# Optimization experiments

Measured on AMD Instinct MI355X. Metric: run time of the kernel, lower is better.

The kernel has to match this reference:

```python
import jax, jax.numpy as jnp
import numpy as np

B = 64            # graphs per batch
NODES_PER_GRAPH = 1008  # 12 snapshots * 84 nodes
N = B * NODES_PER_GRAPH # 64512 total nodes
E = N * 16              # ~1M edges
SNAP = 12
SEG = 84
D_IN = 84
D_H = 128
EPS_BN = 1e-5


def setup_inputs() -> dict:
    key = jax.random.key(0)
    ks = jax.random.split(key, 20)
    s = 0.05  # small init scale for numerical sanity
    return {
        "x": jax.random.normal(ks[0], (N, D_IN), jnp.float32),
        "edge_index": jax.random.randint(ks[1], (2, E), 0, N, jnp.int64),
        "w1": jax.random.normal(ks[2], (D_IN, D_H), jnp.float32) * s,
        "b1": jax.random.normal(ks[3], (D_H,), jnp.float32) * s,
        "w2": jax.random.normal(ks[4], (D_H, D_H), jnp.float32) * s,
        "b2": jax.random.normal(ks[5], (D_H,), jnp.float32) * s,
        "pe": jax.random.normal(ks[6], (NODES_PER_GRAPH, D_H), jnp.float32) * s,
        "wf1": jax.random.normal(ks[7], (SNAP * 4 * D_H, 512), jnp.float32) * s,
        "bf1": jax.random.normal(ks[8], (512,), jnp.float32) * s,
        "g1": jnp.ones((512,), jnp.float32),
        "be1": jnp.zeros((512,), jnp.float32),
        "wf2": jax.random.normal(ks[9], (512, 32), jnp.float32) * s,
        "bf2": jax.random.normal(ks[10], (32,), jnp.float32) * s,
        "g2": jnp.ones((32,), jnp.float32),
        "be2": jnp.zeros((32,), jnp.float32),
        "wf3": jax.random.normal(ks[11], (32, 2), jnp.float32) * s,
        "bf3": jax.random.normal(ks[12], (2,), jnp.float32) * s,
    }


def _batch_norm(h, g, b):
    # training-mode BN: biased batch statistics, eps=1e-5 (torch default)
    mu = jnp.mean(h, axis=0)
    var = jnp.var(h, axis=0)
    return (h - mu) * jax.lax.rsqrt(var + EPS_BN) * g + b


def reference(x, edge_index, w1, b1, w2, b2, pe, wf1, bf1, g1, be1,
              wf2, bf2, g2, be2, wf3, bf3):
    src, dst = edge_index[0], edge_index[1]
    n = x.shape[0]
    b = n // NODES_PER_GRAPH

    # GINConv (eps=0, sum aggregation): h = Linear(x + sum_{j->i} x_j)
    agg1 = jax.ops.segment_sum(x[src], dst, num_segments=n)
    h1 = (x + agg1) @ w1 + b1                      # [N,128]
    agg2 = jax.ops.segment_sum(h1[src], dst, num_segments=n)
    h2 = (h1 + agg2) @ w2 + b2                     # [N,128]

    # positional encoding + full self-attention per graph (1008 tokens)
    h2 = h2.reshape(b, NODES_PER_GRAPH, D_H) + pe  # [B,1008,128]
    score = jnp.einsum('bqd,bkd->bqk', h2, h2) / np.sqrt(float(D_H))
    attn = jax.nn.softmax(score, axis=-1)
    ctx = jnp.einsum('bqk,bkd->bqd', attn, h2)     # [B,1008,128]

    # segmented max/mean pooling: blocks of 84 nodes, 12 snapshots per graph
    h1s = h1.reshape(b, SNAP, SEG, D_H)
    h2s = ctx.reshape(b, SNAP, SEG, D_H)
    feat = jnp.concatenate([
        jnp.max(h1s, axis=2), jnp.mean(h1s, axis=2),
        jnp.max(h2s, axis=2), jnp.mean(h2s, axis=2),
    ], axis=-1)                                    # [B,12,512]
    feat = feat.reshape(b, SNAP * 4 * D_H)         # [B,6144]

    # MLP head (dropout = identity at eval; BN in training-stat mode)
    out = _batch_norm(jax.nn.silu(feat @ wf1 + bf1), g1, be1)
    out = _batch_norm(jax.nn.silu(out @ wf2 + bf2), g2, be2)
    out = jax.nn.softmax(out @ wf3 + bf3, axis=1)  # [B,2]
    return out
```

## Files before the change

### kernel.cpp

```cpp
#include <hip/hip_runtime.h>
#include <math.h>

#define N_NODES 64512
#define DIN 84
#define XHP 96
#define KP 96
#define USP 104
#define DH 128
#define NPG 1008
#define BG 64
#define NSNAP 12
#define NSEG 84
#define NEDGE (N_NODES * 16)
#define DEGCAP 64
#define NBUCK 252
#define EPB 4096
#define BCAP 4608
#define ATT_SCALE 0.08838834764831845f

typedef __bf16 bf16_t;
typedef __bf16 bf16x8 __attribute__((ext_vector_type(8)));
typedef __bf16 bf16x4 __attribute__((ext_vector_type(4)));
typedef float f32x4 __attribute__((ext_vector_type(4)));
typedef _Float16 f16_t;
typedef _Float16 f16x4 __attribute__((ext_vector_type(4)));
typedef _Float16 f16x8 __attribute__((ext_vector_type(8)));

__device__ __forceinline__ f32x4 up4(f16x4 v) {
    return (f32x4){(float)v[0], (float)v[1], (float)v[2], (float)v[3]};
}

__global__ __launch_bounds__(256) void cvt_xh(const float* __restrict__ x,
                                              f16_t* __restrict__ xh,
                                              int* __restrict__ bucketTail) {
    int t = blockIdx.x * 256 + threadIdx.x;
    if (t < N_NODES * 21) {
        int node = t / 21;
        int c = t - node * 21;
        f32x4 v = *(const f32x4*)(x + (size_t)node * DIN + c * 4);
        f16x4 o;
        o[0] = (f16_t)v[0]; o[1] = (f16_t)v[1];
        o[2] = (f16_t)v[2]; o[3] = (f16_t)v[3];
        *(f16x4*)(xh + (size_t)node * XHP + c * 4) = o;
    }
    if (t * 4 < NBUCK) {
        int4 z = {0, 0, 0, 0};
        *(int4*)(bucketTail + t * 4) = z;
    }
}

__global__ __launch_bounds__(256) void epart(const int* __restrict__ src,
                                             const int* __restrict__ dst,
                                             int* __restrict__ bucketTail,
                                             unsigned int* __restrict__ rec) {
    __shared__ int lcnt[NBUCK];
    __shared__ int gbase[NBUCK];
    int tid = threadIdx.x;
    int e0 = blockIdx.x * EPB;
    for (int i = tid; i < NBUCK; i += 256) lcnt[i] = 0;
    __syncthreads();

    unsigned int r[16];
    unsigned short lp[16];
    unsigned short bk[16];
#pragma unroll
    for (int i = 0; i < 16; i++) {
        int e = e0 + tid + i * 256;
        int s = src[e], d = dst[e];
        r[i] = ((unsigned int)d << 16) | (unsigned int)s;
        int b = d >> 8;
        bk[i] = (unsigned short)b;
        lp[i] = (unsigned short)atomicAdd(&lcnt[b], 1);
    }
    __syncthreads();
    for (int i = tid; i < NBUCK; i += 256)
        gbase[i] = atomicAdd(&bucketTail[i], lcnt[i]);
    __syncthreads();
#pragma unroll
    for (int i = 0; i < 16; i++) {
        int b = bk[i];
        int g = gbase[b] + lp[i];
        if (g < BCAP) rec[(size_t)b * BCAP + g] = r[i];
    }
}

__global__ __launch_bounds__(256) void ebuild(const unsigned int* __restrict__ rec,
                                              const int* __restrict__ bucketTail,
                                              int* __restrict__ cnt,
                                              unsigned short* __restrict__ eidx) {
    __shared__ unsigned short stage[256 * 72];
    __shared__ int rb8[256 * 8];
    int tid = threadIdx.x;
    int b = blockIdx.x;
#pragma unroll
    for (int i = 0; i < 8; i++) rb8[tid + i * 256] = 0;
    __syncthreads();

    int n = min(bucketTail[b], BCAP);
    const unsigned int* rbp = rec + (size_t)b * BCAP;
    for (int i = tid; i < n; i += 256) {
        unsigned int rv = rbp[i];
        int ld = (rv >> 16) & 255;
        int rng = (rv & 0xffffu) >> 13;
        atomicAdd(&rb8[ld * 8 + rng], 1);
    }
    __syncthreads();
    {
        int s = 0;
#pragma unroll
        for (int r = 0; r < 8; r++) {
            int c = rb8[tid * 8 + r];
            rb8[tid * 8 + r] = s;
            s += c;
        }
        cnt[b * 256 + tid] = s;
    }
    __syncthreads();
    for (int i = tid; i < n; i += 256) {
        unsigned int rv = rbp[i];
        int ld = (rv >> 16) & 255;
        int rng = (rv & 0xffffu) >> 13;
        int p = atomicAdd(&rb8[ld * 8 + rng], 1);
        if (p < DEGCAP) stage[ld * 72 + p] = (unsigned short)(rv & 0xffffu);
    }
    __syncthreads();

    uint4* op = (uint4*)(eidx + (size_t)b * 256 * DEGCAP);
#pragma unroll
    for (int i = 0; i < 8; i++) {
        int ch = tid + i * 256;
        int node = ch >> 3, e0 = (ch & 7) << 3;
        op[ch] = *(const uint4*)&stage[node * 72 + e0];
    }
}

__global__ __launch_bounds__(128) void prep_w12(const float* __restrict__ w1,
                                                const float* __restrict__ w2,
                                                const float* __restrict__ b1,
                                                f16_t* __restrict__ w1hT,
                                                f16_t* __restrict__ w12hT,
                                                float* __restrict__ bvec) {
    __shared__ float rowv[DH];
    int r = blockIdx.x;
    int j = threadIdx.x;
    const float* srcv = (r < DIN) ? (w1 + (size_t)r * DH) : b1;
    rowv[j] = srcv[j];
    __syncthreads();
    float acc = 0.f;
#pragma unroll 4
    for (int k = 0; k < DH; k++) acc += rowv[k] * w2[k * DH + j];
    if (r < DIN) {
        w12hT[j * KP + r] = (f16_t)acc;
        w1hT[j * KP + r] = (f16_t)w1[(size_t)r * DH + j];
    } else {
        bvec[j] = acc;
        for (int k = DIN; k < KP; k++) {
            w1hT[j * KP + k] = (f16_t)0.f;
            w12hT[j * KP + k] = (f16_t)0.f;
        }
    }
}

__global__ __launch_bounds__(512) void gin1(const float* __restrict__ x,
                                            const f16_t* __restrict__ xh,
                                            const int* __restrict__ cnt,
                                            const unsigned short* __restrict__ eidx,
                                            const f16_t* __restrict__ w1hT,
                                            const float* __restrict__ b1,
                                            float* __restrict__ h1,
                                            f16_t* __restrict__ zh) {
    __shared__ f16_t us[32][USP];
    int n0 = blockIdx.x * 32;
    int tid = threadIdx.x;
    int grp = tid >> 4;
    int gl = tid & 15;
    int node = n0 + grp;
    int s = node * DEGCAP;
    int e = s + min(cnt[node], DEGCAP);
    bool has2 = gl < 5;

    const float* xn = x + (size_t)node * DIN;
    f32x4 a0 = *(const f32x4*)(xn + gl * 4);
    f32x4 a1 = has2 ? *(const f32x4*)(xn + 64 + gl * 4) : (f32x4){0.f, 0.f, 0.f, 0.f};

    int i = s;
    for (; i + 4 <= e; i += 4) {
        const f16_t* p0 = xh + (size_t)eidx[i] * XHP + gl * 4;
        const f16_t* p1 = xh + (size_t)eidx[i + 1] * XHP + gl * 4;
        const f16_t* p2 = xh + (size_t)eidx[i + 2] * XHP + gl * 4;
        const f16_t* p3 = xh + (size_t)eidx[i + 3] * XHP + gl * 4;
        a0 += up4(*(const f16x4*)p0) + up4(*(const f16x4*)p1) +
              up4(*(const f16x4*)p2) + up4(*(const f16x4*)p3);
        if (has2) {
            a1 += up4(*(const f16x4*)(p0 + 64)) + up4(*(const f16x4*)(p1 + 64)) +
                  up4(*(const f16x4*)(p2 + 64)) + up4(*(const f16x4*)(p3 + 64));
        }
    }
    for (; i < e; i++) {
        const f16_t* p0 = xh + (size_t)eidx[i] * XHP + gl * 4;
        a0 += up4(*(const f16x4*)p0);
        if (has2) a1 += up4(*(const f16x4*)(p0 + 64));
    }

    f16x4 z0;
    z0[0] = (f16_t)a0[0]; z0[1] = (f16_t)a0[1];
    z0[2] = (f16_t)a0[2]; z0[3] = (f16_t)a0[3];
    *(f16x4*)(zh + (size_t)node * XHP + gl * 4) = z0;
    *(f16x4*)&us[grp][gl * 4] = z0;
    if (has2) {
        f16x4 z1;
        z1[0] = (f16_t)a1[0]; z1[1] = (f16_t)a1[1];
        z1[2] = (f16_t)a1[2]; z1[3] = (f16_t)a1[3];
        *(f16x4*)(zh + (size_t)node * XHP + 64 + gl * 4) = z1;
        *(f16x4*)&us[grp][64 + gl * 4] = z1;
    }
    if (gl >= 5 && gl < 8) {
        f16x4 zz = {(f16_t)0.f, (f16_t)0.f, (f16_t)0.f, (f16_t)0.f};
        *(f16x4*)&us[grp][64 + gl * 4] = zz;
    }
    __syncthreads();

    int wv = tid >> 6, lane = tid & 63;
    int l15 = lane & 15, quad = lane >> 4;
    int dim = wv * 16 + l15;
    f32x4 acc[2];
    acc[0] = (f32x4){0.f, 0.f, 0.f, 0.f};
    acc[1] = (f32x4){0.f, 0.f, 0.f, 0.f};
#pragma unroll
    for (int ks = 0; ks < 3; ks++) {
        f16x8 bW = *(const f16x8*)(w1hT + (size_t)dim * KP + ks * 32 + quad * 8);
        f16x8 aU0 = *(const f16x8*)&us[l15][ks * 32 + quad * 8];
        f16x8 aU1 = *(const f16x8*)&us[16 + l15][ks * 32 + quad * 8];
        acc[0] = __builtin_amdgcn_mfma_f32_16x16x32_f16(aU0, bW, acc[0], 0, 0, 0);
        acc[1] = __builtin_amdgcn_mfma_f32_16x16x32_f16(aU1, bW, acc[1], 0, 0, 0);
    }
    float bias = b1[dim];
#pragma unroll
    for (int tm = 0; tm < 2; tm++) {
        int nb = n0 + tm * 16 + quad * 4;
#pragma unroll
        for (int r = 0; r < 4; r++)
            h1[(size_t)(nb + r) * DH + dim] = acc[tm][r] + bias;
    }
}

__global__ __launch_bounds__(512) void gin2(const f16_t* __restrict__ zh,
                                            const int* __restrict__ cnt,
                                            const unsigned short* __restrict__ eidx,
                                            const f16_t* __restrict__ w12hT,
                                            const float* __restrict__ bvec,
                                            const float* __restrict__ b2,
                                            const float* __restrict__ pe,
                                            bf16_t* __restrict__ h2bf,
                                            bf16_t* __restrict__ h2T) {
    __shared__ f16_t us[32][USP];
    __shared__ float sdeg[32];
    int n0 = blockIdx.x * 32;
    int tid = threadIdx.x;
    int grp = tid >> 4;
    int gl = tid & 15;
    int node = n0 + grp;
    int dg = min(cnt[node], DEGCAP);
    int s = node * DEGCAP;
    int e = s + dg;
    bool has2 = gl < 5;
    if (gl == 0) sdeg[grp] = (float)(1 + dg);

    const f16_t* zn = zh + (size_t)node * XHP;
    f32x4 a0 = up4(*(const f16x4*)(zn + gl * 4));
    f32x4 a1 = has2 ? up4(*(const f16x4*)(zn + 64 + gl * 4)) : (f32x4){0.f, 0.f, 0.f, 0.f};

    int i = s;
    for (; i + 4 <= e; i += 4) {
        const f16_t* p0 = zh + (size_t)eidx[i] * XHP + gl * 4;
        const f16_t* p1 = zh + (size_t)eidx[i + 1] * XHP + gl * 4;
        const f16_t* p2 = zh + (size_t)eidx[i + 2] * XHP + gl * 4;
        const f16_t* p3 = zh + (size_t)eidx[i + 3] * XHP + gl * 4;
        a0 += up4(*(const f16x4*)p0) + up4(*(const f16x4*)p1) +
              up4(*(const f16x4*)p2) + up4(*(const f16x4*)p3);
        if (has2) {
            a1 += up4(*(const f16x4*)(p0 + 64)) + up4(*(const f16x4*)(p1 + 64)) +
                  up4(*(const f16x4*)(p2 + 64)) + up4(*(const f16x4*)(p3 + 64));
        }
    }
    for (; i < e; i++) {
        const f16_t* p0 = zh + (size_t)eidx[i] * XHP + gl * 4;
        a0 += up4(*(const f16x4*)p0);
        if (has2) a1 += up4(*(const f16x4*)(p0 + 64));
    }
    f16x4 u0;
    u0[0] = (f16_t)a0[0]; u0[1] = (f16_t)a0[1];
    u0[2] = (f16_t)a0[2]; u0[3] = (f16_t)a0[3];
    *(f16x4*)&us[grp][gl * 4] = u0;
    if (has2) {
        f16x4 u1;
        u1[0] = (f16_t)a1[0]; u1[1] = (f16_t)a1[1];
        u1[2] = (f16_t)a1[2]; u1[3] = (f16_t)a1[3];
        *(f16x4*)&us[grp][64 + gl * 4] = u1;
    }
    if (gl >= 5 && gl < 8) {
        f16x4 zz = {(f16_t)0.f, (f16_t)0.f, (f16_t)0.f, (f16_t)0.f};
        *(f16x4*)&us[grp][64 + gl * 4] = zz;
    }
    __syncthreads();

    int wv = tid >> 6, lane = tid & 63;
    int l15 = lane & 15, quad = lane >> 4;
    int dim = wv * 16 + l15;
    f32x4 acc[2];
    acc[0] = (f32x4){0.f, 0.f, 0.f, 0.f};
    acc[1] = (f32x4){0.f, 0.f, 0.f, 0.f};
#pragma unroll
    for (int ks = 0; ks < 3; ks++) {
        f16x8 bW = *(const f16x8*)(w12hT + (size_t)dim * KP + ks * 32 + quad * 8);
        f16x8 aU0 = *(const f16x8*)&us[l15][ks * 32 + quad * 8];
        f16x8 aU1 = *(const f16x8*)&us[16 + l15][ks * 32 + quad * 8];
        acc[0] = __builtin_amdgcn_mfma_f32_16x16x32_f16(aU0, bW, acc[0], 0, 0, 0);
        acc[1] = __builtin_amdgcn_mfma_f32_16x16x32_f16(aU1, bW, acc[1], 0, 0, 0);
    }

    float bb = b2[dim];
    float bv = bvec[dim];
#pragma unroll
    for (int tm = 0; tm < 2; tm++) {
        int nb = n0 + tm * 16 + quad * 4;
        int bg = nb / NPG;
        int pos = nb - bg * NPG;
        bf16x4 tv;
#pragma unroll
        for (int r = 0; r < 4; r++) {
            float v = acc[tm][r] + bb + sdeg[tm * 16 + quad * 4 + r] * bv +
                      pe[(size_t)(pos + r) * DH + dim];
            bf16_t vb = (bf16_t)v;
            h2bf[(size_t)(nb + r) * DH + dim] = vb;
            tv[r] = vb;
        }
        *(bf16x4*)(h2T + ((size_t)bg * DH + dim) * NPG + pos) = tv;
    }
}

#define QTILE 256
#define KTILE 64
#define KS_PITCH 152
#define KT_PITCH 88
#define PS_PITCH 88
#define KSSZ 9728
#define KTSZ 11264
#define BUFSZ (KSSZ + KTSZ)
#define PS2_OFF (2 * BUFSZ)

__global__ __launch_bounds__(512, 1) void attn_mfma(const bf16_t* __restrict__ h2bf,
                                                    const bf16_t* __restrict__ h2T,
                                                    float* __restrict__ ctx) {
    __shared__ __align__(16) bf16_t smem[PS2_OFF + QTILE * PS_PITCH];

    int tid = threadIdx.x;
    int wv = tid >> 6, lane = tid & 63;
    int l15 = lane & 15, quad = lane >> 4;
    int idx = blockIdx.x;
    int xcd = idx & 7;
    int qt = (idx >> 3) & 3;
    int b = (idx >> 5) * 8 + xcd;
    const bf16_t* hb = h2bf + (size_t)b * NPG * DH;
    const bf16_t* hbT = h2T + (size_t)b * DH * NPG;

    bf16x8 bQ[2][4];
#pragma unroll
    for (int set = 0; set < 2; set++) {
        int qrow_frag = qt * QTILE + wv * 32 + set * 16 + l15;
        int qsrc = (qrow_frag < NPG) ? qrow_frag : 0;
#pragma unroll
        for (int kb = 0; kb < 4; kb++)
            bQ[set][kb] = *(const bf16x8*)(hb + (size_t)qsrc * DH + kb * 32 + quad * 8);
    }

    float m0 = -1e30f, li0 = 0.0f;
    float m1 = -1e30f, li1 = 0.0f;
    f32x4 O[2][8];
#pragma unroll
    for (int t = 0; t < 8; t++) {
        O[0][t] = (f32x4){0.f, 0.f, 0.f, 0.f};
        O[1][t] = (f32x4){0.f, 0.f, 0.f, 0.f};
    }

    uint4 rK[2], rT[2];
#define LOADR(KT_)                                                              \
    {                                                                           \
        int kt_ = (KT_);                                                        \
        _Pragma("unroll")                                                       \
        for (int i = 0; i < 2; i++) {                                           \
            int c = tid + i * 512;                                              \
            int row = c >> 4, seg = c & 15;                                     \
            int key = kt_ * KTILE + row;                                        \
            uint4 v = {0u, 0u, 0u, 0u};                                         \
            if (key < NPG) v = *(const uint4*)(hb + (size_t)key * DH + seg * 8);\
            rK[i] = v;                                                          \
        }                                                                       \
        _Pragma("unroll")                                                       \
        for (int i = 0; i < 2; i++) {                                           \
            int c = tid + i * 512;                                              \
            int dim = c >> 3, kc = c & 7;                                       \
            int key0 = kt_ * KTILE + kc * 8;                                    \
            uint4 v = {0u, 0u, 0u, 0u};                                         \
            if (key0 < NPG) v = *(const uint4*)(hbT + (size_t)dim * NPG + key0);\
            rT[i] = v;                                                          \
        }                                                                       \
    }
#define DRAIN(BUFOFF_)                                                          \
    {                                                                           \
        int bo_ = (BUFOFF_);                                                    \
        _Pragma("unroll")                                                       \
        for (int i = 0; i < 2; i++) {                                           \
            int c = tid + i * 512;                                              \
            int row = c >> 4, seg = c & 15;                                     \
            *(uint4*)&smem[bo_ + row * KS_PITCH + seg * 8] = rK[i];             \
        }                                                                       \
        _Pragma("unroll")                                                       \
        for (int i = 0; i < 2; i++) {                                           \
            int c = tid + i * 512;                                              \
            int dim = c >> 3, kc = c & 7;                                       \
            *(uint4*)&smem[bo_ + KSSZ + dim * KT_PITCH + kc * 8] = rT[i];       \
        }                                                                       \
    }

    LOADR(0);
    DRAIN(0);
    LOADR(1);
    __syncthreads();

    for (int kt = 0; kt < 16; kt++) {
        int bo = (kt & 1) * BUFSZ;
        if (kt < 15) DRAIN(((kt + 1) & 1) * BUFSZ);
        if (kt < 14) LOADR(kt + 2);

        f32x4 S[2][4];
#pragma unroll
        for (int nt = 0; nt < 4; nt++) {
            S[0][nt] = (f32x4){0.f, 0.f, 0.f, 0.f};
            S[1][nt] = (f32x4){0.f, 0.f, 0.f, 0.f};
#pragma unroll
            for (int kb = 0; kb < 4; kb++) {
                bf16x8 aK = *(const bf16x8*)&smem[bo + (nt * 16 + l15) * KS_PITCH + kb * 32 + quad * 8];
                S[0][nt] = __builtin_amdgcn_mfma_f32_16x16x32_bf16(aK, bQ[0][kb], S[0][nt], 0, 0, 0);
                S[1][nt] = __builtin_amdgcn_mfma_f32_16x16x32_bf16(aK, bQ[1][kb], S[1][nt], 0, 0, 0);
            }
        }

        float pmax0 = -1e30f, pmax1 = -1e30f;
#pragma unroll
        for (int nt = 0; nt < 4; nt++) {
            bool valid = (kt * KTILE + nt * 16) < NPG;
#pragma unroll
            for (int r = 0; r < 4; r++) {
                float v0 = valid ? S[0][nt][r] * ATT_SCALE : -1e30f;
                float v1 = valid ? S[1][nt][r] * ATT_SCALE : -1e30f;
                S[0][nt][r] = v0;
                S[1][nt][r] = v1;
                pmax0 = fmaxf(pmax0, v0);
                pmax1 = fmaxf(pmax1, v1);
            }
        }
        pmax0 = fmaxf(pmax0, __shfl_xor(pmax0, 16));
        pmax0 = fmaxf(pmax0, __shfl_xor(pmax0, 32));
        pmax1 = fmaxf(pmax1, __shfl_xor(pmax1, 16));
        pmax1 = fmaxf(pmax1, __shfl_xor(pmax1, 32));
        float newm0 = fmaxf(m0, pmax0);
        float newm1 = fmaxf(m1, pmax1);

        float alpha0 = 1.0f, alpha1 = 1.0f;
        if (!__all((newm0 == m0) && (newm1 == m1))) {
            alpha0 = __expf(m0 - newm0);
            alpha1 = __expf(m1 - newm1);
            float a00 = __shfl(alpha0, quad * 4 + 0);
            float a01 = __shfl(alpha0, quad * 4 + 1);
            float a02 = __shfl(alpha0, quad * 4 + 2);
            float a03 = __shfl(alpha0, quad * 4 + 3);
            float a10 = __shfl(alpha1, quad * 4 + 0);
            float a11 = __shfl(alpha1, quad * 4 + 1);
            float a12 = __shfl(alpha1, quad * 4 + 2);
            float a13 = __shfl(alpha1, quad * 4 + 3);
#pragma unroll
            for (int t = 0; t < 8; t++) {
                O[0][t][0] *= a00; O[0][t][1] *= a01; O[0][t][2] *= a02; O[0][t][3] *= a03;
                O[1][t][0] *= a10; O[1][t][1] *= a11; O[1][t][2] *= a12; O[1][t][3] *= a13;
            }
        }
        m0 = newm0;
        m1 = newm1;

        float psum0 = 0.f, psum1 = 0.f;
#pragma unroll
        for (int nt = 0; nt < 4; nt++) {
            bf16x4 pk0, pk1;
#pragma unroll
            for (int r = 0; r < 4; r++) {
                float p0 = __expf(S[0][nt][r] - newm0);
                float p1 = __expf(S[1][nt][r] - newm1);
                psum0 += p0;
                psum1 += p1;
                pk0[r] = (bf16_t)p0;
                pk1[r] = (bf16_t)p1;
            }
            *(bf16x4*)&smem[PS2_OFF + (wv * 32 + l15) * PS_PITCH + nt * 16 + quad * 4] = pk0;
            *(bf16x4*)&smem[PS2_OFF + (wv * 32 + 16 + l15) * PS_PITCH + nt * 16 + quad * 4] = pk1;
        }
        psum0 += __shfl_xor(psum0, 16);
        psum0 += __shfl_xor(psum0, 32);
        psum1 += __shfl_xor(psum1, 16);
        psum1 += __shfl_xor(psum1, 32);
        li0 = li0 * alpha0 + psum0;
        li1 = li1 * alpha1 + psum1;

#pragma unroll
        for (int kb2 = 0; kb2 < 2; kb2++) {
            bf16x8 aP0 = *(const bf16x8*)&smem[PS2_OFF + (wv * 32 + l15) * PS_PITCH + kb2 * 32 + quad * 8];
            bf16x8 aP1 = *(const bf16x8*)&smem[PS2_OFF + (wv * 32 + 16 + l15) * PS_PITCH + kb2 * 32 + quad * 8];
#pragma unroll
            for (int t = 0; t < 8; t++) {
                bf16x8 bV = *(const bf16x8*)&smem[bo + KSSZ + (t * 16 + l15) * KT_PITCH + kb2 * 32 + quad * 8];
                O[0][t] = __builtin_amdgcn_mfma_f32_16x16x32_bf16(aP0, bV, O[0][t], 0, 0, 0);
                O[1][t] = __builtin_amdgcn_mfma_f32_16x16x32_bf16(aP1, bV, O[1][t], 0, 0, 0);
            }
        }

        __syncthreads();
    }
#undef LOADR
#undef DRAIN

    float invl0[4], invl1[4];
#pragma unroll
    for (int r = 0; r < 4; r++) {
        invl0[r] = 1.0f / __shfl(li0, quad * 4 + r);
        invl1[r] = 1.0f / __shfl(li1, quad * 4 + r);
    }
    float* cb = ctx + (size_t)b * NPG * DH;
#pragma unroll
    for (int t = 0; t < 8; t++)
#pragma unroll
        for (int r = 0; r < 4; r++) {
            int qrow0 = qt * QTILE + wv * 32 + quad * 4 + r;
            int qrow1 = qrow0 + 16;
            if (qrow0 < NPG) cb[(size_t)qrow0 * DH + t * 16 + l15] = O[0][t][r] * invl0[r];
            if (qrow1 < NPG) cb[(size_t)qrow1 * DH + t * 16 + l15] = O[1][t][r] * invl1[r];
        }
}

__global__ __launch_bounds__(128) void pooling(const float* __restrict__ h1,
                                               const float* __restrict__ ctx,
                                               const float* __restrict__ bf1,
                                               float* __restrict__ feat,
                                               float* __restrict__ y1raw) {
    int bs = blockIdx.x;
    int d = threadIdx.x;
    if (bs < 256) {
        int i = bs * 128 + d;
        y1raw[i] = bf1[i & 511];
    }
    int base = bs * NSEG;
    float mx1 = -1e30f, sm1 = 0.f, mx2 = -1e30f, sm2 = 0.f;
    for (int n = 0; n < NSEG; n++) {
        float v1 = h1[(size_t)(base + n) * DH + d];
        mx1 = fmaxf(mx1, v1);
        sm1 += v1;
        float v2 = ctx[(size_t)(base + n) * DH + d];
        mx2 = fmaxf(mx2, v2);
        sm2 += v2;
    }
    const float invs = 1.0f / NSEG;
    feat[bs * 512 + d] = mx1;
    feat[bs * 512 + 128 + d] = sm1 * invs;
    feat[bs * 512 + 256 + d] = mx2;
    feat[bs * 512 + 384 + d] = sm2 * invs;
}

#define MLP1_KCH 96
__global__ __launch_bounds__(256) void mlp1_splitk(const float* __restrict__ feat,
                                                   const float* __restrict__ wf1,
                                                   float* __restrict__ y1raw) {
    __shared__ float fl[64][MLP1_KCH];
    int k0 = blockIdx.y * MLP1_KCH;
    int tid = threadIdx.x;
    for (int c = tid; c < 64 * MLP1_KCH; c += 256) {
        int row = c / MLP1_KCH;
        int kk = c - row * MLP1_KCH;
        fl[row][kk] = feat[(size_t)row * 6144 + k0 + kk];
    }
    __syncthreads();
    int col = blockIdx.x * 128 + (tid & 127);
    int rbase = (tid >> 7) * 32;
    float acc[32];
#pragma unroll
    for (int r = 0; r < 32; r++) acc[r] = 0.f;
    for (int kg = 0; kg < MLP1_KCH; kg += 4) {
        float w0 = wf1[(size_t)(k0 + kg + 0) * 512 + col];
        float w1 = wf1[(size_t)(k0 + kg + 1) * 512 + col];
        float w2 = wf1[(size_t)(k0 + kg + 2) * 512 + col];
        float w3 = wf1[(size_t)(k0 + kg + 3) * 512 + col];
#pragma unroll
        for (int r = 0; r < 32; r++) {
            float4 f = *(const float4*)&fl[rbase + r][kg];
            acc[r] += f.x * w0 + f.y * w1 + f.z * w2 + f.w * w3;
        }
    }
#pragma unroll
    for (int r = 0; r < 32; r++)
        atomicAdd(&y1raw[(size_t)(rbase + r) * 512 + col], acc[r]);
}

__global__ __launch_bounds__(1024) void head_tail(const float* __restrict__ y1raw,
                                                  const float* __restrict__ g1,
                                                  const float* __restrict__ be1,
                                                  const float* __restrict__ wf2,
                                                  const float* __restrict__ bf2,
                                                  const float* __restrict__ g2,
                                                  const float* __restrict__ be2,
                                                  const float* __restrict__ wf3,
                                                  const float* __restrict__ bf3,
                                                  float* __restrict__ out) {
    __shared__ float sscale[512];
    __shared__ float sshift[512];
    __shared__ float zsm[64][68];
    __shared__ float y2sm[64][33];
    __shared__ float scale2[32], shift2[32];

    int tid = threadIdx.x;

    if (tid < 512) {
        float s = 0.f, s2 = 0.f;
        for (int b = 0; b < 64; b++) {
            float v = y1raw[b * 512 + tid];
            float h = v / (1.0f + __expf(-v));
            s += h;
            s2 += h * h;
        }
        float mu = s * (1.0f / 64.0f);
        float var = s2 * (1.0f / 64.0f) - mu * mu;
        float sc = rsqrtf(var + 1e-5f) * g1[tid];
        sscale[tid] = sc;
        sshift[tid] = be1[tid] - mu * sc;
    }
    __syncthreads();

    int b0 = tid >> 5;
    int b1 = b0 + 32;
    int j2 = tid & 31;
    float acc0 = bf2[j2], acc1 = acc0;
    for (int kc = 0; kc < 8; kc++) {
        __syncthreads();
#pragma unroll
        for (int c = 0; c < 4; c++) {
            int lin = tid + c * 1024;
            int bb = lin >> 6;
            int kk = lin & 63;
            int k = kc * 64 + kk;
            float v = y1raw[bb * 512 + k];
            float h = v / (1.0f + __expf(-v));
            zsm[bb][kk] = h * sscale[k] + sshift[k];
        }
        __syncthreads();
        for (int kk = 0; kk < 64; kk++) {
            float wv = wf2[(kc * 64 + kk) * 32 + j2];
            acc0 += zsm[b0][kk] * wv;
            acc1 += zsm[b1][kk] * wv;
        }
    }
    y2sm[b0][j2] = acc0;
    y2sm[b1][j2] = acc1;
    __syncthreads();

    if (tid < 32) {
        float s = 0.f, s2 = 0.f;
        for (int b = 0; b < 64; b++) {
            float h = y2sm[b][tid];
            float hs = h / (1.0f + __expf(-h));
            s += hs;
            s2 += hs * hs;
        }
        float mu = s * (1.0f / 64.0f);
        float var = s2 * (1.0f / 64.0f) - mu * mu;
        float sc = rsqrtf(var + 1e-5f) * g2[tid];
        scale2[tid] = sc;
        shift2[tid] = be2[tid] - mu * sc;
    }
    __syncthreads();

    if (tid < 64) {
        float l0 = bf3[0], l1 = bf3[1];
        for (int k = 0; k < 32; k++) {
            float h = y2sm[tid][k];
            float hs = h / (1.0f + __expf(-h));
            float v = hs * scale2[k] + shift2[k];
            l0 += v * wf3[k * 2 + 0];
            l1 += v * wf3[k * 2 + 1];
        }
        float m = fmaxf(l0, l1);
        float e0 = __expf(l0 - m), e1 = __expf(l1 - m);
        float inv = 1.0f / (e0 + e1);
        out[tid * 2 + 0] = e0 * inv;
        out[tid * 2 + 1] = e1 * inv;
    }
}

extern "C" void kernel_launch(void* const* d_in, const int* in_sizes, int n_in,
                              void* d_out, int out_size, void* d_ws, size_t ws_size,
                              hipStream_t stream) {
    const float* x   = (const float*)d_in[0];
    const int*   ei  = (const int*)d_in[1];
    const float* w1  = (const float*)d_in[2];
    const float* b1  = (const float*)d_in[3];
    const float* w2  = (const float*)d_in[4];
    const float* b2  = (const float*)d_in[5];
    const float* pe  = (const float*)d_in[6];
    const float* wf1 = (const float*)d_in[7];
    const float* bf1 = (const float*)d_in[8];
    const float* g1  = (const float*)d_in[9];
    const float* be1 = (const float*)d_in[10];
    const float* wf2 = (const float*)d_in[11];
    const float* bf2 = (const float*)d_in[12];
    const float* g2  = (const float*)d_in[13];
    const float* be2 = (const float*)d_in[14];
    const float* wf3 = (const float*)d_in[15];
    const float* bf3 = (const float*)d_in[16];
    float* out = (float*)d_out;

    const int* srcp = ei;
    const int* dstp = ei + NEDGE;

    float* ws = (float*)d_ws;
    size_t off = 0;
    float* h1   = ws + off; off += (size_t)N_NODES * DH;
    float* ctxb = ws + off; off += (size_t)N_NODES * DH;
    float* feat = ws + off; off += (size_t)BG * NSNAP * 512;
    bf16_t* h2bf = (bf16_t*)(ws + off); off += (size_t)N_NODES * DH / 2;
    bf16_t* h2T  = (bf16_t*)(ws + off); off += (size_t)N_NODES * DH / 2;
    f16_t* zh    = (f16_t*)(ws + off);  off += (size_t)N_NODES * XHP / 2;
    f16_t* xh    = (f16_t*)(ws + off);  off += (size_t)N_NODES * XHP / 2;
    float* y1raw = ws + off; off += 64 * 512;
    f16_t* w1hT  = (f16_t*)(ws + off);  off += (size_t)DH * KP / 2;
    f16_t* w12hT = (f16_t*)(ws + off);  off += (size_t)DH * KP / 2;
    float* bvec  = ws + off; off += DH;
    int* bucketTail = (int*)(ws + off); off += NBUCK;
    int* cnt  = (int*)(ws + off); off += N_NODES;
    unsigned int* rec = (unsigned int*)(ws + off); off += (size_t)NBUCK * BCAP;
    unsigned short* eidx = (unsigned short*)(ws + off);

    cvt_xh<<<(N_NODES * 21 + 255) / 256, 256, 0, stream>>>(x, xh, bucketTail);
    prep_w12<<<DIN + 1, 128, 0, stream>>>(w1, w2, b1, w1hT, w12hT, bvec);
    epart<<<NEDGE / EPB, 256, 0, stream>>>(srcp, dstp, bucketTail, rec);
    ebuild<<<NBUCK, 256, 0, stream>>>(rec, bucketTail, cnt, eidx);

    gin1<<<N_NODES / 32, 512, 0, stream>>>(x, xh, cnt, eidx, w1hT, b1, h1, zh);
    gin2<<<N_NODES / 32, 512, 0, stream>>>(zh, cnt, eidx, w12hT, bvec, b2, pe, h2bf, h2T);
    attn_mfma<<<BG * 4, 512, 0, stream>>>(h2bf, h2T, ctxb);
    pooling<<<BG * NSNAP, 128, 0, stream>>>(h1, ctxb, bf1, feat, y1raw);
    mlp1_splitk<<<dim3(4, 64), 256, 0, stream>>>(feat, wf1, y1raw);
    head_tail<<<1, 1024, 0, stream>>>(y1raw, g1, be1, wf2, bf2, g2, be2, wf3, bf3, out);
}
```

Measured before the change: 360.8 us.

## Split single-block MLP head into BN-stats, per-row MLP2, and tail kernels

The single 1024-thread head kernel is replaced by three kernels. One computes the first BN scale and shift over 4 blocks. One runs the 512x32 layer with one block per batch row. The last does the second BN and softmax. This spreads the serial head work across more CUs, at the cost of two extra kernel launches and global round-trips for the intermediate scale, shift and y2 buffers.

```diff
diff --git a/kernel.cpp b/kernel.cpp
--- a/kernel.cpp
+++ b/kernel.cpp
@@ -608,65 +608,70 @@
         atomicAdd(&y1raw[(size_t)(rbase + r) * 512 + col], acc[r]);
 }
 
-__global__ __launch_bounds__(1024) void head_tail(const float* __restrict__ y1raw,
-                                                  const float* __restrict__ g1,
-                                                  const float* __restrict__ be1,
-                                                  const float* __restrict__ wf2,
-                                                  const float* __restrict__ bf2,
-                                                  const float* __restrict__ g2,
-                                                  const float* __restrict__ be2,
-                                                  const float* __restrict__ wf3,
-                                                  const float* __restrict__ bf3,
-                                                  float* __restrict__ out) {
-    __shared__ float sscale[512];
-    __shared__ float sshift[512];
-    __shared__ float zsm[64][68];
+__global__ __launch_bounds__(128) void bn1s(const float* __restrict__ y1raw,
+                                            const float* __restrict__ g1,
+                                            const float* __restrict__ be1,
+                                            float* __restrict__ sscale,
+                                            float* __restrict__ sshift) {
+    int f = blockIdx.x * 128 + threadIdx.x;
+    float s = 0.f, s2 = 0.f;
+#pragma unroll 8
+    for (int b = 0; b < 64; b++) {
+        float v = y1raw[b * 512 + f];
+        float h = v / (1.0f + __expf(-v));
+        s += h;
+        s2 += h * h;
+    }
+    float mu = s * (1.0f / 64.0f);
+    float var = s2 * (1.0f / 64.0f) - mu * mu;
+    float sc = rsqrtf(var + 1e-5f) * g1[f];
+    sscale[f] = sc;
+    sshift[f] = be1[f] - mu * sc;
+}
+
+__global__ __launch_bounds__(256) void mlp2k(const float* __restrict__ y1raw,
+                                             const float* __restrict__ sscale,
+                                             const float* __restrict__ sshift,
+                                             const float* __restrict__ wf2,
+                                             const float* __restrict__ bf2,
+                                             float* __restrict__ y2raw) {
+    __shared__ float zrow[512];
+    __shared__ float part[8][33];
+    int b = blockIdx.x;
+    int tid = threadIdx.x;
+    for (int k = tid; k < 512; k += 256) {
+        float v = y1raw[b * 512 + k];
+        float h = v / (1.0f + __expf(-v));
+        zrow[k] = h * sscale[k] + sshift[k];
+    }
+    __syncthreads();
+    int j = tid & 31, s = tid >> 5;
+    float acc = 0.f;
+    int k0 = s * 64;
+#pragma unroll 8
+    for (int k = 0; k < 64; k++)
+        acc += zrow[k0 + k] * wf2[(k0 + k) * 32 + j];
+    part[s][j] = acc;
+    __syncthreads();
+    if (tid < 32) {
+        float a = bf2[tid];
+#pragma unroll
+        for (int ss = 0; ss < 8; ss++) a += part[ss][tid];
+        y2raw[b * 32 + tid] = a;
+    }
+}
+
+__global__ __launch_bounds__(256) void tail(const float* __restrict__ y2raw,
+                                            const float* __restrict__ g2,
+                                            const float* __restrict__ be2,
+                                            const float* __restrict__ wf3,
+                                            const float* __restrict__ bf3,
+                                            float* __restrict__ out) {
     __shared__ float y2sm[64][33];
     __shared__ float scale2[32], shift2[32];
-
     int tid = threadIdx.x;
-
-    if (tid < 512) {
-        float s = 0.f, s2 = 0.f;
-        for (int b = 0; b < 64; b++) {
-            float v = y1raw[b * 512 + tid];
-            float h = v / (1.0f + __expf(-v));
-            s += h;
-            s2 += h * h;
-        }
-        float mu = s * (1.0f / 64.0f);
-        float var = s2 * (1.0f / 64.0f) - mu * mu;
-        float sc = rsqrtf(var + 1e-5f) * g1[tid];
-        sscale[tid] = sc;
-        sshift[tid] = be1[tid] - mu * sc;
-    }
-    __syncthreads();
-
-    int b0 = tid >> 5;
-    int b1 = b0 + 32;
-    int j2 = tid & 31;
-    float acc0 = bf2[j2], acc1 = acc0;
-    for (int kc = 0; kc < 8; kc++) {
-        __syncthreads();
-#pragma unroll
-        for (int c = 0; c < 4; c++) {
-            int lin = tid + c * 1024;
-            int bb = lin >> 6;
-            int kk = lin & 63;
-            int k = kc * 64 + kk;
-            float v = y1raw[bb * 512 + k];
-            float h = v / (1.0f + __expf(-v));
-            zsm[bb][kk] = h * sscale[k] + sshift[k];
-        }
-        __syncthreads();
-        for (int kk = 0; kk < 64; kk++) {
-            float wv = wf2[(kc * 64 + kk) * 32 + j2];
-            acc0 += zsm[b0][kk] * wv;
-            acc1 += zsm[b1][kk] * wv;
-        }
-    }
-    y2sm[b0][j2] = acc0;
-    y2sm[b1][j2] = acc1;
+    for (int i = tid; i < 64 * 32; i += 256)
+        y2sm[i >> 5][i & 31] = y2raw[i];
     __syncthreads();
 
     if (tid < 32) {
@@ -737,6 +742,9 @@
     f16_t* zh    = (f16_t*)(ws + off);  off += (size_t)N_NODES * XHP / 2;
     f16_t* xh    = (f16_t*)(ws + off);  off += (size_t)N_NODES * XHP / 2;
     float* y1raw = ws + off; off += 64 * 512;
+    float* sscale = ws + off; off += 512;
+    float* sshift = ws + off; off += 512;
+    float* y2raw  = ws + off; off += 64 * 32;
     f16_t* w1hT  = (f16_t*)(ws + off);  off += (size_t)DH * KP / 2;
     f16_t* w12hT = (f16_t*)(ws + off);  off += (size_t)DH * KP / 2;
     float* bvec  = ws + off; off += DH;
@@ -755,5 +763,7 @@
     attn_mfma<<<BG * 4, 512, 0, stream>>>(h2bf, h2T, ctxb);
     pooling<<<BG * NSNAP, 128, 0, stream>>>(h1, ctxb, bf1, feat, y1raw);
     mlp1_splitk<<<dim3(4, 64), 256, 0, stream>>>(feat, wf1, y1raw);
-    head_tail<<<1, 1024, 0, stream>>>(y1raw, g1, be1, wf2, bf2, g2, be2, wf3, bf3, out);
-}
+    bn1s<<<4, 128, 0, stream>>>(y1raw, g1, be1, sscale, sshift);
+    mlp2k<<<64, 256, 0, stream>>>(y1raw, sscale, sshift, wf2, bf2, y2raw);
+    tail<<<1, 256, 0, stream>>>(y2raw, g2, be2, wf3, bf3, out);
+}
```

Result: faster. 339.5 us (-5.9%).
